# Kernel optimization log

Measured on AMD Instinct MI355X. Metric: run time of the kernel, lower is better.

Reference implementation:

```python
import jax, jax.numpy as jnp
import numpy as np

C = 256
D = C // 8  # query/key channels


def setup_inputs() -> dict:
    key = jax.random.key(0)
    ks = jax.random.split(key, 7)
    x = jax.random.normal(ks[0], (4, C, 64, 64), dtype=jnp.float32)
    s1 = 1.0 / np.sqrt(C)
    w1 = jax.random.normal(ks[1], (D, C), dtype=jnp.float32) * s1
    b1 = jax.random.normal(ks[2], (D,), dtype=jnp.float32) * 0.01
    w2 = jax.random.normal(ks[3], (D, C), dtype=jnp.float32) * s1
    b2 = jax.random.normal(ks[4], (D,), dtype=jnp.float32) * 0.01
    w3 = jax.random.normal(ks[5], (C, C), dtype=jnp.float32) * s1
    b3 = jax.random.normal(ks[6], (C,), dtype=jnp.float32) * 0.01
    return {"x": x, "w1": w1, "b1": b1, "w2": w2, "b2": b2, "w3": w3, "b3": b3}


def reference(x, w1, b1, w2, b2, w3, b3):
    B, Cc, W, H = x.shape
    N = W * H
    xf = x.reshape(B, Cc, N)  # [B, C, N] flattened spatial
    # 1x1 convs are per-pixel linear maps over channels
    q = jnp.einsum('dc,bcn->bnd', w1, xf) + b1  # [B, N, D]
    k = jnp.einsum('dc,bcn->bdn', w2, xf) + b2[:, None]  # [B, D, N]
    v = jnp.einsum('oc,bcn->bon', w3, xf) + b3[:, None]  # [B, C, N]
    energy = jnp.einsum('bnd,bdm->bnm', q, k)  # [B, N, N]
    attn = jax.nn.softmax(energy, axis=-1)
    out = jnp.einsum('bcm,bnm->bcn', v, attn)  # bmm(V, attn^T)
    out = out.reshape(B, Cc, W, H) + x
    return out
```

## Files before the change

### kernel.cpp

```cpp
#include <hip/hip_runtime.h>
#include <hip/hip_fp16.h>

typedef _Float16 half8 __attribute__((ext_vector_type(8)));
typedef float f32x16 __attribute__((ext_vector_type(16)));
typedef float f32x4v __attribute__((ext_vector_type(4)));

#define MFMA16(A, B, C) __builtin_amdgcn_mfma_f32_32x32x16_f16((A), (B), (C), 0, 0, 0)

__device__ __forceinline__ f32x16 fzero16() {
  f32x16 z;
#pragma unroll
  for (int i = 0; i < 16; ++i) z[i] = 0.0f;
  return z;
}

struct HiLo { _Float16 hi, lo; };
__device__ __forceinline__ HiLo split1(float f) {
  HiLo r;
  r.hi = (_Float16)f;
  r.lo = (_Float16)(f - (float)r.hi);
  return r;
}

__global__ __launch_bounds__(256) void wprep_kernel(
    const float* __restrict__ w1, const float* __restrict__ w2,
    const float* __restrict__ w3,
    _Float16* __restrict__ w1p, _Float16* __restrict__ w2p,
    _Float16* __restrict__ w3p)
{
  const int t = threadIdx.x;
  const int blk = blockIdx.x;
  if (blk < 8) {
    const int cot = blk;
    for (int e = t; e < 8192; e += 256) {
      const int j = e & 7, l = (e >> 3) & 63, cs = e >> 9;
      const int lr = l & 31, h = l >> 5;
      const int row = cot * 32 + lr;
      const int col = cs * 16 + 4 * h + (j & 3) + 8 * (j >> 2);
      const HiLo s = split1(w3[row * 256 + col]);
      const int idx = ((cot * 16 + cs) * 64 + l) * 8 + j;
      w3p[idx] = s.hi;
      w3p[65536 + idx] = s.lo;
    }
  } else {
    for (int e = t; e < 8192; e += 256) {
      const int j = e & 7, l = (e >> 3) & 63, cs = e >> 9;
      const int lr = l & 31, h = l >> 5;
      const int col = cs * 16 + 4 * h + (j & 3) + 8 * (j >> 2);
      const HiLo s1 = split1(w1[lr * 256 + col]);
      const HiLo s2 = split1(w2[lr * 256 + col]);
      const int idx = (cs * 64 + l) * 8 + j;
      w1p[idx] = s1.hi; w1p[8192 + idx] = s1.lo;
      w2p[idx] = s2.hi; w2p[8192 + idx] = s2.lo;
    }
  }
}

__global__ __launch_bounds__(256) void qkv_proj_kernel(
    const float* __restrict__ x,
    const _Float16* __restrict__ w1p, const float* __restrict__ b1,
    const _Float16* __restrict__ w2p, const float* __restrict__ b2,
    const _Float16* __restrict__ w3p, const float* __restrict__ b3,
    _Float16* __restrict__ qb, _Float16* __restrict__ kb,
    _Float16* __restrict__ vb)
{
  __shared__ f32x4v red[4][2][4][64];
  const int t = threadIdx.x, w = t >> 6, l = t & 63;
  const int lr = l & 31, h = l >> 5;
  const int b = blockIdx.x >> 7;
  const int nt = blockIdx.x & 127;
  const float* xb = x + (size_t)b * 256 * 4096 + nt * 32 + lr;
  const int cot0 = w * 2, cot1 = w * 2 + 1;

  f32x16 accq = fzero16(), acck = fzero16();
  f32x16 accv0 = fzero16(), accv1 = fzero16();

  for (int cs = 0; cs < 16; ++cs) {
    const int c0 = cs * 16 + 4 * h;
    half8 xh, xl;
#pragma unroll
    for (int j = 0; j < 8; ++j) {
      const int c = c0 + (j & 3) + 8 * (j >> 2);
      const HiLo s = split1(xb[(size_t)c * 4096]);
      xh[j] = s.hi; xl[j] = s.lo;
    }
    const half8 wh0 = *(const half8*)&w3p[((cot0 * 16 + cs) * 64 + l) * 8];
    const half8 wl0 = *(const half8*)&w3p[65536 + ((cot0 * 16 + cs) * 64 + l) * 8];
    const half8 wh1 = *(const half8*)&w3p[((cot1 * 16 + cs) * 64 + l) * 8];
    const half8 wl1 = *(const half8*)&w3p[65536 + ((cot1 * 16 + cs) * 64 + l) * 8];
    accv0 = MFMA16(xh, wh0, accv0);
    accv0 = MFMA16(xl, wh0, accv0);
    accv0 = MFMA16(xh, wl0, accv0);
    accv1 = MFMA16(xh, wh1, accv1);
    accv1 = MFMA16(xl, wh1, accv1);
    accv1 = MFMA16(xh, wl1, accv1);
    if ((cs >> 2) == w) {
      const half8 w1h = *(const half8*)&w1p[(cs * 64 + l) * 8];
      const half8 w1l = *(const half8*)&w1p[8192 + (cs * 64 + l) * 8];
      const half8 w2h = *(const half8*)&w2p[(cs * 64 + l) * 8];
      const half8 w2l = *(const half8*)&w2p[8192 + (cs * 64 + l) * 8];
      accq = MFMA16(w1h, xh, accq);
      accq = MFMA16(w1h, xl, accq);
      accq = MFMA16(w1l, xh, accq);
      acck = MFMA16(w2h, xh, acck);
      acck = MFMA16(w2h, xl, acck);
      acck = MFMA16(w2l, xh, acck);
    }
  }

  const float bv0 = b3[cot0 * 32 + lr];
  const float bv1 = b3[cot1 * 32 + lr];
#pragma unroll
  for (int hfq = 0; hfq < 2; ++hfq) {
    half8 p0, p1;
#pragma unroll
    for (int j = 0; j < 8; ++j) {
      p0[j] = (_Float16)(accv0[8 * hfq + j] + bv0);
      p1[j] = (_Float16)(accv1[8 * hfq + j] + bv1);
    }
    const int ms = nt * 2 + hfq;
    *(half8*)&vb[((((size_t)b * 256 + ms) * 8 + cot0) * 64 + l) * 8] = p0;
    *(half8*)&vb[((((size_t)b * 256 + ms) * 8 + cot1) * 64 + l) * 8] = p1;
  }

#pragma unroll
  for (int i4 = 0; i4 < 4; ++i4) {
    f32x4v q4, k4;
#pragma unroll
    for (int c = 0; c < 4; ++c) { q4[c] = accq[4 * i4 + c]; k4[c] = acck[4 * i4 + c]; }
    red[w][0][i4][l] = q4;
    red[w][1][i4][l] = k4;
  }
  __syncthreads();
  if (w < 2) {
    _Float16* dst = (w == 0) ? qb : kb;
    const float* bias = (w == 0) ? b1 : b2;
    f32x16 tot;
#pragma unroll
    for (int i4 = 0; i4 < 4; ++i4) {
      f32x4v v = red[0][w][i4][l];
      v += red[1][w][i4][l];
      v += red[2][w][i4][l];
      v += red[3][w][i4][l];
#pragma unroll
      for (int c = 0; c < 4; ++c) tot[4 * i4 + c] = v[c];
    }
#pragma unroll
    for (int ds = 0; ds < 2; ++ds) {
      half8 ph;
#pragma unroll
      for (int j = 0; j < 8; ++j) {
        const int d = 16 * ds + 4 * h + (j & 3) + 8 * (j >> 2);
        ph[j] = (_Float16)(tot[8 * ds + j] + bias[d]);
      }
      *(half8*)&dst[((((size_t)b * 128 + nt) * 2 + ds) * 64 + l) * 8] = ph;
    }
  }
}

__device__ __forceinline__ float max16(float vm, const f32x16& s) {
  const float g1 = fmaxf(fmaxf(s[0], s[1]), s[2]);
  const float g2 = fmaxf(fmaxf(s[3], s[4]), s[5]);
  const float g3 = fmaxf(fmaxf(s[6], s[7]), s[8]);
  const float g4 = fmaxf(fmaxf(s[9], s[10]), s[11]);
  const float g5 = fmaxf(fmaxf(s[12], s[13]), s[14]);
  const float h1 = fmaxf(fmaxf(g1, g2), g3);
  const float h2 = fmaxf(fmaxf(g4, g5), s[15]);
  return fmaxf(fmaxf(vm, h1), h2);
}

__global__ __launch_bounds__(512) void rowmax_kernel(
    const _Float16* __restrict__ qb, const _Float16* __restrict__ kb,
    float* __restrict__ Mrow)
{
  __shared__ float red[2][8][32];
  const int t = threadIdx.x, w = t >> 6, l = t & 63;
  const int bid = blockIdx.x;
  const int xcd = bid & 7;
  const int b = xcd >> 1;
  const int sp = ((bid >> 3) << 1) | (xcd & 1);
  const int sl0 = sp * 2, sl1 = sp * 2 + 1;
  const _Float16* qp0 = qb + ((((size_t)b * 128 + sl0) * 2) * 64 + l) * 8;
  const _Float16* qp1 = qb + ((((size_t)b * 128 + sl1) * 2) * 64 + l) * 8;
  const half8 q00 = *(const half8*)qp0;
  const half8 q01 = *(const half8*)(qp0 + 512);
  const half8 q10 = *(const half8*)qp1;
  const half8 q11 = *(const half8*)(qp1 + 512);
  float vm0 = -3.0e38f, vm1 = -3.0e38f;
  for (int mt = w * 16; mt < w * 16 + 16; ++mt) {
    const _Float16* kp = kb + ((((size_t)b * 128 + mt) * 2) * 64 + l) * 8;
    const half8 k0 = *(const half8*)kp;
    const half8 k1 = *(const half8*)(kp + 512);
    f32x16 s0 = fzero16();
    s0 = MFMA16(k0, q00, s0);
    s0 = MFMA16(k1, q01, s0);
    f32x16 s1 = fzero16();
    s1 = MFMA16(k0, q10, s1);
    s1 = MFMA16(k1, q11, s1);
    vm0 = max16(vm0, s0);
    vm1 = max16(vm1, s1);
  }
  vm0 = fmaxf(vm0, __shfl_xor(vm0, 32));
  vm1 = fmaxf(vm1, __shfl_xor(vm1, 32));
  if (l < 32) { red[0][w][l] = vm0; red[1][w][l] = vm1; }
  __syncthreads();
  if (t < 64) {
    const int slab = t >> 5, r = t & 31;
    float m = red[slab][0][r];
#pragma unroll
    for (int ww = 1; ww < 8; ++ww) m = fmaxf(m, red[slab][ww][r]);
    Mrow[(size_t)b * 4096 + (sp * 2 + slab) * 32 + r] = m;
  }
}

__global__ __launch_bounds__(512, 1) void attn_kernel(
    const _Float16* __restrict__ qb, const _Float16* __restrict__ kb,
    const _Float16* __restrict__ vb, const float* __restrict__ Mrow,
    const float* __restrict__ x, float* __restrict__ out)
{
  __shared__ __align__(16) _Float16 Plds[2][2][2][8][64][8];
  __shared__ float Lred[2][4][32];
  const int t = threadIdx.x, w = t >> 6, l = t & 63;
  const int lr = l & 31, h = l >> 5;
  const int bid = blockIdx.x;
  const int xcd = bid & 7;
  const int b = xcd >> 1;
  const int rg = ((bid >> 3) << 1) | (xcd & 1);
  const int sw = w >> 2;
  const int kq = w & 3;

  const _Float16* kbase = kb + (size_t)b * 131072 + (size_t)l * 8;
  const _Float16* vbase = vb + (size_t)b * 1048576 + (size_t)w * 512 + (size_t)l * 8;

#define KF(kt, ds) (*(const half8*)(kbase + ((size_t)(((kt) * 4 + kq) * 2 + (ds))) * 512))
#define VF(kt, ks) (*(const half8*)(vbase + ((size_t)(((kt) * 8 + (ks)) * 8)) * 512))

  const int rt32q = rg * 2 + sw;
  const _Float16* qp = qb + (((size_t)b * 128 + rt32q) * 2 * 64 + l) * 8;
  const half8 qf0 = *(const half8*)qp;
  const half8 qf1 = *(const half8*)(qp + 512);
  const float LOG2E = 1.44269504088896340736f;
  const float Mr = Mrow[(size_t)b * 4096 + rt32q * 32 + lr];
  const float nM2 = -Mr * LOG2E;

  f32x16 acc0 = fzero16(), acc1 = fzero16();
  float Lacc = 0.f;
  half8 va0[8], va1[8];
  half8 ka0, ka1, kb0_, kb1_;

#define EXPPACK(S, BUF, TI)                                                    \
  {                                                                            \
    float pvv[16];                                                             \
    float ls = 0.f;                                                            \
    _Pragma("unroll") for (int i = 0; i < 16; ++i) {                           \
      pvv[i] = exp2f(fmaf((S)[i], LOG2E, nM2)); ls += pvv[i];                  \
    }                                                                          \
    Lacc += ls;                                                                \
    half8 ph0, ph1;                                                            \
    _Pragma("unroll") for (int jj = 0; jj < 4; ++jj) {                         \
      auto a0 = __builtin_amdgcn_cvt_pkrtz(pvv[2 * jj], pvv[2 * jj + 1]);      \
      auto a1 = __builtin_amdgcn_cvt_pkrtz(pvv[8 + 2 * jj], pvv[8 + 2 * jj + 1]); \
      ph0[2 * jj] = a0[0]; ph0[2 * jj + 1] = a0[1];                            \
      ph1[2 * jj] = a1[0]; ph1[2 * jj + 1] = a1[1];                            \
    }                                                                          \
    *(half8*)&Plds[BUF][TI][sw][kq * 2 + 0][l][0] = ph0;                       \
    *(half8*)&Plds[BUF][TI][sw][kq * 2 + 1][l][0] = ph1;                       \
  }

#define PVC(CB, TI, VA)                                                        \
  {                                                                            \
    __builtin_amdgcn_s_setprio(1);                                             \
    _Pragma("unroll") for (int ks = 0; ks < 8; ++ks) {                         \
      const half8 pb0 = *(const half8*)&Plds[CB][TI][0][ks][l][0];             \
      const half8 pb1 = *(const half8*)&Plds[CB][TI][1][ks][l][0];             \
      acc0 = MFMA16(VA[ks], pb0, acc0);                                        \
      acc1 = MFMA16(VA[ks], pb1, acc1);                                        \
    }                                                                          \
    __builtin_amdgcn_s_setprio(0);                                             \
  }

#define PRODUCE(P, KC0, KC1, PB, TI)                                           \
  {                                                                            \
    f32x16 s = fzero16();                                                      \
    s = MFMA16(KC0, qf0, s);                                                   \
    s = MFMA16(KC1, qf1, s);                                                   \
    if ((P) + 2 < 32) { KC0 = KF((P) + 2, 0); KC1 = KF((P) + 2, 1); }          \
    EXPPACK(s, PB, TI)                                                         \
  }

#pragma unroll
  for (int ks = 0; ks < 8; ++ks) va0[ks] = VF(0, ks);
#pragma unroll
  for (int ks = 0; ks < 8; ++ks) va1[ks] = VF(1, ks);
  {
    const half8 k00 = KF(0, 0), k01 = KF(0, 1);
    f32x16 s = fzero16();
    s = MFMA16(k00, qf0, s);
    s = MFMA16(k01, qf1, s);
    ka0 = KF(2, 0); ka1 = KF(2, 1);
    EXPPACK(s, 0, 0)
  }
  {
    const half8 k10 = KF(1, 0), k11 = KF(1, 1);
    f32x16 s = fzero16();
    s = MFMA16(k10, qf0, s);
    s = MFMA16(k11, qf1, s);
    kb0_ = KF(3, 0); kb1_ = KF(3, 1);
    EXPPACK(s, 0, 1)
  }
  asm volatile("s_waitcnt lgkmcnt(0)" ::: "memory");
  __builtin_amdgcn_s_barrier();
  asm volatile("" ::: "memory");

  for (int P = 0; P < 16; ++P) {
    const int CB = P & 1, PB = CB ^ 1;
    const int p0 = 2 * P + 2, p1 = 2 * P + 3;

    if (sw == 0) {
      if (p0 < 32) { PRODUCE(p0, ka0, ka1, PB, 0) }
      PVC(CB, 0, va0)
    } else {
      PVC(CB, 0, va0)
      if (p0 < 32) { PRODUCE(p0, ka0, ka1, PB, 0) }
    }
    if (p0 < 32) {
#pragma unroll
      for (int ks = 0; ks < 8; ++ks) va0[ks] = VF(p0, ks);
    }

    if (sw == 0) {
      if (p1 < 32) { PRODUCE(p1, kb0_, kb1_, PB, 1) }
      PVC(CB, 1, va1)
    } else {
      PVC(CB, 1, va1)
      if (p1 < 32) { PRODUCE(p1, kb0_, kb1_, PB, 1) }
    }
    if (p1 < 32) {
#pragma unroll
      for (int ks = 0; ks < 8; ++ks) va1[ks] = VF(p1, ks);
    }

    asm volatile("s_waitcnt lgkmcnt(0)" ::: "memory");
    __builtin_amdgcn_s_barrier();
    asm volatile("" ::: "memory");
  }
#undef PRODUCE
#undef PVC
#undef EXPPACK
#undef KF
#undef VF

  {
    const float l2 = Lacc + __shfl_xor(Lacc, 32);
    if (l < 32) Lred[sw][kq][lr] = l2;
  }
  __syncthreads();
  const float invL0 = 1.0f / (Lred[0][0][lr] + Lred[0][1][lr] + Lred[0][2][lr] + Lred[0][3][lr]);
  const float invL1 = 1.0f / (Lred[1][0][lr] + Lred[1][1][lr] + Lred[1][2][lr] + Lred[1][3][lr]);

  const float* xb = x + (size_t)b * 1048576;
  float* ob = out + (size_t)b * 1048576;
  const int nn0 = rg * 64 + lr;
  const int nn1 = rg * 64 + 32 + lr;
#pragma unroll
  for (int reg = 0; reg < 16; ++reg) {
    const int crel = (reg & 3) + 8 * (reg >> 2) + 4 * h;
    const int cout = w * 32 + crel;
    const size_t o0 = (size_t)cout * 4096 + nn0;
    ob[o0] = acc0[reg] * invL0 + xb[o0];
    const size_t o1 = (size_t)cout * 4096 + nn1;
    ob[o1] = acc1[reg] * invL1 + xb[o1];
  }
}

extern "C" void kernel_launch(void* const* d_in, const int* in_sizes, int n_in,
                              void* d_out, int out_size, void* d_ws, size_t ws_size,
                              hipStream_t stream) {
  const float* x  = (const float*)d_in[0];
  const float* w1 = (const float*)d_in[1];
  const float* b1 = (const float*)d_in[2];
  const float* w2 = (const float*)d_in[3];
  const float* b2 = (const float*)d_in[4];
  const float* w3 = (const float*)d_in[5];
  const float* b3 = (const float*)d_in[6];
  float* out = (float*)d_out;

  char* ws = (char*)d_ws;
  _Float16* qb  = (_Float16*)(ws);
  _Float16* kb  = (_Float16*)(ws + (1u << 20));
  _Float16* vb  = (_Float16*)(ws + (2u << 20));
  float*    Mrow = (float*)(ws + (10u << 20));
  _Float16* w1p = (_Float16*)(ws + (10u << 20) + (64u << 10));
  _Float16* w2p = (_Float16*)(ws + (10u << 20) + (96u << 10));
  _Float16* w3p = (_Float16*)(ws + (10u << 20) + (128u << 10));

  hipLaunchKernelGGL(wprep_kernel, dim3(9), dim3(256), 0, stream,
                     w1, w2, w3, w1p, w2p, w3p);
  hipLaunchKernelGGL(qkv_proj_kernel, dim3(512), dim3(256), 0, stream,
                     x, w1p, b1, w2p, b2, w3p, b3, qb, kb, vb);
  hipLaunchKernelGGL(rowmax_kernel, dim3(256), dim3(512), 0, stream, qb, kb, Mrow);
  hipLaunchKernelGGL(attn_kernel, dim3(256), dim3(512), 0, stream,
                     qb, kb, vb, Mrow, x, out);
}
```

Baseline: 83.33 us.

## Drop hi/lo fp16 split in projections and simplify attention wave ordering

```diff
diff --git a/kernel.cpp b/kernel.cpp
--- a/kernel.cpp
+++ b/kernel.cpp
@@ -2,6 +2,7 @@
 #include <hip/hip_fp16.h>
 
 typedef _Float16 half8 __attribute__((ext_vector_type(8)));
+typedef _Float16 half2v __attribute__((ext_vector_type(2)));
 typedef float f32x16 __attribute__((ext_vector_type(16)));
 typedef float f32x4v __attribute__((ext_vector_type(4)));
 
@@ -12,14 +13,6 @@
 #pragma unroll
   for (int i = 0; i < 16; ++i) z[i] = 0.0f;
   return z;
-}
-
-struct HiLo { _Float16 hi, lo; };
-__device__ __forceinline__ HiLo split1(float f) {
-  HiLo r;
-  r.hi = (_Float16)f;
-  r.lo = (_Float16)(f - (float)r.hi);
-  return r;
 }
 
 __global__ __launch_bounds__(256) void wprep_kernel(
@@ -37,21 +30,16 @@
       const int lr = l & 31, h = l >> 5;
       const int row = cot * 32 + lr;
       const int col = cs * 16 + 4 * h + (j & 3) + 8 * (j >> 2);
-      const HiLo s = split1(w3[row * 256 + col]);
-      const int idx = ((cot * 16 + cs) * 64 + l) * 8 + j;
-      w3p[idx] = s.hi;
-      w3p[65536 + idx] = s.lo;
+      w3p[((cot * 16 + cs) * 64 + l) * 8 + j] = (_Float16)w3[row * 256 + col];
     }
   } else {
     for (int e = t; e < 8192; e += 256) {
       const int j = e & 7, l = (e >> 3) & 63, cs = e >> 9;
       const int lr = l & 31, h = l >> 5;
       const int col = cs * 16 + 4 * h + (j & 3) + 8 * (j >> 2);
-      const HiLo s1 = split1(w1[lr * 256 + col]);
-      const HiLo s2 = split1(w2[lr * 256 + col]);
       const int idx = (cs * 64 + l) * 8 + j;
-      w1p[idx] = s1.hi; w1p[8192 + idx] = s1.lo;
-      w2p[idx] = s2.hi; w2p[8192 + idx] = s2.lo;
+      w1p[idx] = (_Float16)w1[lr * 256 + col];
+      w2p[idx] = (_Float16)w2[lr * 256 + col];
     }
   }
 }
@@ -77,34 +65,21 @@
 
   for (int cs = 0; cs < 16; ++cs) {
     const int c0 = cs * 16 + 4 * h;
-    half8 xh, xl;
+    half8 xh;
 #pragma unroll
     for (int j = 0; j < 8; ++j) {
       const int c = c0 + (j & 3) + 8 * (j >> 2);
-      const HiLo s = split1(xb[(size_t)c * 4096]);
-      xh[j] = s.hi; xl[j] = s.lo;
+      xh[j] = (_Float16)xb[(size_t)c * 4096];
     }
     const half8 wh0 = *(const half8*)&w3p[((cot0 * 16 + cs) * 64 + l) * 8];
-    const half8 wl0 = *(const half8*)&w3p[65536 + ((cot0 * 16 + cs) * 64 + l) * 8];
     const half8 wh1 = *(const half8*)&w3p[((cot1 * 16 + cs) * 64 + l) * 8];
-    const half8 wl1 = *(const half8*)&w3p[65536 + ((cot1 * 16 + cs) * 64 + l) * 8];
     accv0 = MFMA16(xh, wh0, accv0);
-    accv0 = MFMA16(xl, wh0, accv0);
-    accv0 = MFMA16(xh, wl0, accv0);
     accv1 = MFMA16(xh, wh1, accv1);
-    accv1 = MFMA16(xl, wh1, accv1);
-    accv1 = MFMA16(xh, wl1, accv1);
     if ((cs >> 2) == w) {
       const half8 w1h = *(const half8*)&w1p[(cs * 64 + l) * 8];
-      const half8 w1l = *(const half8*)&w1p[8192 + (cs * 64 + l) * 8];
       const half8 w2h = *(const half8*)&w2p[(cs * 64 + l) * 8];
-      const half8 w2l = *(const half8*)&w2p[8192 + (cs * 64 + l) * 8];
       accq = MFMA16(w1h, xh, accq);
-      accq = MFMA16(w1h, xl, accq);
-      accq = MFMA16(w1l, xh, accq);
       acck = MFMA16(w2h, xh, acck);
-      acck = MFMA16(w2h, xl, acck);
-      acck = MFMA16(w2l, xh, acck);
     }
   }
 
@@ -256,15 +231,15 @@
       pvv[i] = exp2f(fmaf((S)[i], LOG2E, nM2)); ls += pvv[i];                  \
     }                                                                          \
     Lacc += ls;                                                                \
-    half8 ph0, ph1;                                                            \
+    union { half8 v; half2v h2[4]; } u0, u1;                                   \
     _Pragma("unroll") for (int jj = 0; jj < 4; ++jj) {                         \
       auto a0 = __builtin_amdgcn_cvt_pkrtz(pvv[2 * jj], pvv[2 * jj + 1]);      \
       auto a1 = __builtin_amdgcn_cvt_pkrtz(pvv[8 + 2 * jj], pvv[8 + 2 * jj + 1]); \
-      ph0[2 * jj] = a0[0]; ph0[2 * jj + 1] = a0[1];                            \
-      ph1[2 * jj] = a1[0]; ph1[2 * jj + 1] = a1[1];                            \
+      u0.h2[jj] = *(half2v*)&a0;                                               \
+      u1.h2[jj] = *(half2v*)&a1;                                               \
     }                                                                          \
-    *(half8*)&Plds[BUF][TI][sw][kq * 2 + 0][l][0] = ph0;                       \
-    *(half8*)&Plds[BUF][TI][sw][kq * 2 + 1][l][0] = ph1;                       \
+    *(half8*)&Plds[BUF][TI][sw][kq * 2 + 0][l][0] = u0.v;                      \
+    *(half8*)&Plds[BUF][TI][sw][kq * 2 + 1][l][0] = u1.v;                      \
   }
 
 #define PVC(CB, TI, VA)                                                        \
@@ -279,15 +254,6 @@
     __builtin_amdgcn_s_setprio(0);                                             \
   }
 
-#define PRODUCE(P, KC0, KC1, PB, TI)                                           \
-  {                                                                            \
-    f32x16 s = fzero16();                                                      \
-    s = MFMA16(KC0, qf0, s);                                                   \
-    s = MFMA16(KC1, qf1, s);                                                   \
-    if ((P) + 2 < 32) { KC0 = KF((P) + 2, 0); KC1 = KF((P) + 2, 1); }          \
-    EXPPACK(s, PB, TI)                                                         \
-  }
-
 #pragma unroll
   for (int ks = 0; ks < 8; ++ks) va0[ks] = VF(0, ks);
 #pragma unroll
@@ -316,25 +282,27 @@
     const int CB = P & 1, PB = CB ^ 1;
     const int p0 = 2 * P + 2, p1 = 2 * P + 3;
 
-    if (sw == 0) {
-      if (p0 < 32) { PRODUCE(p0, ka0, ka1, PB, 0) }
-      PVC(CB, 0, va0)
-    } else {
-      PVC(CB, 0, va0)
-      if (p0 < 32) { PRODUCE(p0, ka0, ka1, PB, 0) }
-    }
     if (p0 < 32) {
+      f32x16 s = fzero16();
+      s = MFMA16(ka0, qf0, s);
+      s = MFMA16(ka1, qf1, s);
+      if (p0 + 2 < 32) { ka0 = KF(p0 + 2, 0); ka1 = KF(p0 + 2, 1); }
+      EXPPACK(s, PB, 0)
+    }
+    PVC(CB, 0, va0)
+    if (p0 < 32) {
 #pragma unroll
       for (int ks = 0; ks < 8; ++ks) va0[ks] = VF(p0, ks);
     }
 
-    if (sw == 0) {
-      if (p1 < 32) { PRODUCE(p1, kb0_, kb1_, PB, 1) }
-      PVC(CB, 1, va1)
-    } else {
-      PVC(CB, 1, va1)
-      if (p1 < 32) { PRODUCE(p1, kb0_, kb1_, PB, 1) }
-    }
+    if (p1 < 32) {
+      f32x16 s = fzero16();
+      s = MFMA16(kb0_, qf0, s);
+      s = MFMA16(kb1_, qf1, s);
+      if (p1 + 2 < 32) { kb0_ = KF(p1 + 2, 0); kb1_ = KF(p1 + 2, 1); }
+      EXPPACK(s, PB, 1)
+    }
+    PVC(CB, 1, va1)
     if (p1 < 32) {
 #pragma unroll
       for (int ks = 0; ks < 8; ++ks) va1[ks] = VF(p1, ks);
@@ -344,7 +312,6 @@
     __builtin_amdgcn_s_barrier();
     asm volatile("" ::: "memory");
   }
-#undef PRODUCE
 #undef PVC
 #undef EXPPACK
 #undef KF
```

After: 74.21 us. 1.12x faster.
